# Performance work log

Measured on AMD Instinct MI355X. Metric: run time of the kernel, lower is better.

The kernel has to match this reference:

```python
import jax, jax.numpy as jnp
import numpy as np

B, T, F, H1, H2 = 256, 512, 64, 128, 64


def lstm_seq(x, Wk, Wr, b):
    """Keras-style LSTM with activation='relu', recurrent_activation='sigmoid'.
    x: [B, T, Din]. Returns (all hidden states [B, T, H], last hidden [B, H]).
    Gate order in fused weights is (i, f, g, o) as in Keras."""
    H = Wr.shape[0]
    xT = jnp.swapaxes(x, 0, 1)  # [T, B, Din]
    h0 = jnp.zeros((x.shape[0], H), x.dtype)
    c0 = jnp.zeros((x.shape[0], H), x.dtype)

    def step(carry, xt):
        h, c = carry
        z = xt @ Wk + h @ Wr + b  # [B, 4H]
        i, f, g, o = jnp.split(z, 4, axis=-1)
        i = jax.nn.sigmoid(i)
        f = jax.nn.sigmoid(f)
        o = jax.nn.sigmoid(o)
        g = jax.nn.relu(g)  # activation='relu' replaces tanh
        c = f * c + i * g
        h = o * jax.nn.relu(c)  # relu also applied to cell state output
        return (h, c), h

    (h_last, _), hs = jax.lax.scan(step, (h0, c0), xT)
    return jnp.swapaxes(hs, 0, 1), h_last


def setup_inputs() -> dict:
    key = jax.random.key(0)
    ks = jax.random.split(key, 16)

    def p(k, shape):
        # small init to keep the relu recurrence numerically stable over T=512 steps
        fan_in = shape[0]
        return jax.random.normal(k, shape, dtype=jnp.float32) * (0.5 / np.sqrt(fan_in))

    inp = {
        "x": jax.random.normal(ks[0], (B, T, F), dtype=jnp.float32),
        # encoder layer 1: F -> H1
        "Wk1": p(ks[1], (F, 4 * H1)), "Wr1": p(ks[2], (H1, 4 * H1)), "b1": jnp.zeros((4 * H1,), jnp.float32),
        # encoder layer 2: H1 -> H2 (return last state only)
        "Wk2": p(ks[3], (H1, 4 * H2)), "Wr2": p(ks[4], (H2, 4 * H2)), "b2": jnp.zeros((4 * H2,), jnp.float32),
        # decoder layer 1: H2 -> H2
        "Wd1k": p(ks[5], (H2, 4 * H2)), "Wd1r": p(ks[6], (H2, 4 * H2)), "bd1": jnp.zeros((4 * H2,), jnp.float32),
        # decoder layer 2: H2 -> H1
        "Wd2k": p(ks[7], (H2, 4 * H1)), "Wd2r": p(ks[8], (H1, 4 * H1)), "bd2": jnp.zeros((4 * H1,), jnp.float32),
        # TimeDistributed Dense: H1 -> F
        "Wout": p(ks[9], (H1, F)), "bout": jnp.zeros((F,), jnp.float32),
    }
    return inp


def reference(x, Wk1, Wr1, b1, Wk2, Wr2, b2, Wd1k, Wd1r, bd1, Wd2k, Wd2r, bd2, Wout, bout):
    # Encoder
    h_seq, _ = lstm_seq(x, Wk1, Wr1, b1)            # [B, T, H1]
    _, z = lstm_seq(h_seq, Wk2, Wr2, b2)            # [B, H2] (return_sequences=False)
    # RepeatVector
    z_rep = jnp.broadcast_to(z[:, None, :], (z.shape[0], T, z.shape[1]))  # [B, T, H2]
    # Decoder
    d1, _ = lstm_seq(z_rep, Wd1k, Wd1r, bd1)        # [B, T, H2]
    d2, _ = lstm_seq(d1, Wd2k, Wd2r, bd2)           # [B, T, H1]
    # TimeDistributed Dense
    return d2 @ Wout + bout                          # [B, T, F]
```

## Files before the change

kernel.cpp:

```cpp
#include <hip/hip_runtime.h>

static constexpr int TT = 512;
static constexpr int BB = 256;

#define BARRIER() do { \
    asm volatile("s_waitcnt lgkmcnt(0)" ::: "memory"); \
    __builtin_amdgcn_s_barrier(); \
    asm volatile("" ::: "memory"); \
  } while (0)

__device__ __forceinline__ float sigmoid_fast(float v) {
  const float e = __builtin_amdgcn_exp2f(v * -1.44269504088896340736f);
  return __builtin_amdgcn_rcpf(1.0f + e);
}

__device__ __forceinline__ float dpp_add_xor1(float v) {
  const int p = __builtin_amdgcn_update_dpp(0, __builtin_bit_cast(int, v),
                                            0xB1 , 0xF, 0xF, true);
  return v + __builtin_bit_cast(float, p);
}
__device__ __forceinline__ float dpp_add_xor2(float v) {
  const int p = __builtin_amdgcn_update_dpp(0, __builtin_bit_cast(int, v),
                                            0x4E , 0xF, 0xF, true);
  return v + __builtin_bit_cast(float, p);
}
__device__ __forceinline__ float swz_add_xor4(float v) {
  const int p = __builtin_amdgcn_ds_swizzle(__builtin_bit_cast(int, v), 0x101F);
  return v + __builtin_bit_cast(float, p);
}

template<int DIN, int H, int NSu, bool CONST_X, bool WRITE_SEQ, bool WRITE_LAST, bool FUSE_DENSE>
__global__ void __launch_bounds__(512, 2)
lstm_unit(const float* __restrict__ xin,
          const float* __restrict__ Wk,
          const float* __restrict__ Wr,
          const float* __restrict__ bias,
          float* __restrict__ seq_out,
          float* __restrict__ last_out,
          const float* __restrict__ Wout,
          const float* __restrict__ boutp,
          float* __restrict__ dense_out)
{
  constexpr int NTH  = 512;
  static_assert(H * NSu == NTH, "block = H*NSu = 512");
  constexpr int KTOT = DIN + H;
  constexpr int SL   = KTOT / NSu;
  constexpr int C4H  = 4 * H;
  constexpr int XH   = DIN + H;
  constexpr int NW   = NTH / 64;
  constexpr int UPW  = 64 / NSu;
  constexpr int DK   = FUSE_DENSE ? (H / NW) : 4;
  static_assert(SL * NSu == KTOT && (SL % 4) == 0, "slice float4-able");
  static_assert(NSu == 4 || NSu == 8, "butterfly depth");

  const int tid = (int)threadIdx.x;
  const int b   = (int)blockIdx.x;
  const int l   = tid & 63;
  const int wv  = tid >> 6;
  const int sl  = l & (NSu - 1);
  const int u   = wv * UPW + (l / NSu);

  __shared__ __align__(16) float xh0[XH], xh1[XH];
  __shared__ __align__(16) float dp[2][FUSE_DENSE ? NW * 64 : 4];

  float w[SL * 4];
  #pragma unroll
  for (int i = 0; i < SL; ++i) {
    const int k = sl * SL + i;
    const float* col = (k < DIN) ? &Wk[(size_t)k * C4H] : &Wr[(size_t)(k - DIN) * C4H];
    #pragma unroll
    for (int g = 0; g < 4; ++g) w[i * 4 + g] = col[g * H + u];
  }
  const float bi_ = bias[u], bf_ = bias[H + u], bg_ = bias[2 * H + u], bo_ = bias[3 * H + u];

  float wout_r[DK];
  float boutr = 0.f;
  if constexpr (FUSE_DENSE) {
    #pragma unroll
    for (int j = 0; j < DK; ++j) wout_r[j] = Wout[(size_t)(DK * wv + j) * 64 + l];
    boutr = boutp[l];
  }

  if (tid < H) xh0[DIN + tid] = 0.f;
  if (tid < DIN / 4) {
    const float4 v = *(const float4*)&xin[(CONST_X ? (size_t)b * DIN
                                                   : (size_t)b * TT * DIN) + 4 * tid];
    *((float4*)xh0 + tid) = v;
    if (CONST_X) *((float4*)xh1 + tid) = v;
  }
  BARRIER();

  float cst = 0.f;
  constexpr int TEND = FUSE_DENSE ? TT + 2 : TT;

  for (int t = 0; t < TEND; ++t) {
    float* xc = (t & 1) ? xh1 : xh0;
    float* xn = (t & 1) ? xh0 : xh1;

    float4 xr;
    const bool do_stage = (!CONST_X) && (tid < DIN / 4) && (t + 1 < TT);
    if (do_stage) xr = *(const float4*)&xin[((size_t)b * TT + (t + 1)) * DIN + 4 * tid];

    if (t < TT) {
      const float4* xv = (const float4*)(xc + sl * SL);
      float ai = 0.f, af = 0.f, ag = 0.f, ao = 0.f;
      #pragma unroll
      for (int j = 0; j < SL / 4; ++j) {
        const float4 v = xv[j];
        const float* wj = &w[16 * j];
        ai = fmaf(v.x, wj[0],  ai);  af = fmaf(v.x, wj[1],  af);
        ag = fmaf(v.x, wj[2],  ag);  ao = fmaf(v.x, wj[3],  ao);
        ai = fmaf(v.y, wj[4],  ai);  af = fmaf(v.y, wj[5],  af);
        ag = fmaf(v.y, wj[6],  ag);  ao = fmaf(v.y, wj[7],  ao);
        ai = fmaf(v.z, wj[8],  ai);  af = fmaf(v.z, wj[9],  af);
        ag = fmaf(v.z, wj[10], ag);  ao = fmaf(v.z, wj[11], ao);
        ai = fmaf(v.w, wj[12], ai);  af = fmaf(v.w, wj[13], af);
        ag = fmaf(v.w, wj[14], ag);  ao = fmaf(v.w, wj[15], ao);
      }
      ai = dpp_add_xor1(ai); af = dpp_add_xor1(af);
      ag = dpp_add_xor1(ag); ao = dpp_add_xor1(ao);
      ai = dpp_add_xor2(ai); af = dpp_add_xor2(af);
      ag = dpp_add_xor2(ag); ao = dpp_add_xor2(ao);
      if constexpr (NSu == 8) {
        ai = swz_add_xor4(ai); af = swz_add_xor4(af);
        ag = swz_add_xor4(ag); ao = swz_add_xor4(ao);
      }
      const float gi = sigmoid_fast(ai + bi_);
      const float gf = sigmoid_fast(af + bf_);
      const float go = sigmoid_fast(ao + bo_);
      const float gg = fmaxf(ag + bg_, 0.f);
      cst = fmaf(gf, cst, gi * gg);
      const float h = go * fmaxf(cst, 0.f);
      if (sl == 0) {
        xn[DIN + u] = h;
        if constexpr (WRITE_SEQ)  seq_out[((size_t)b * TT + t) * H + u] = h;
        if constexpr (WRITE_LAST) { if (t == TT - 1) last_out[(size_t)b * H + u] = h; }
      }
    }
    if (do_stage) *((float4*)xn + tid) = xr;

    if constexpr (FUSE_DENSE) {
      if (t >= 1 && t <= TT) {
        const float* hsrc = xc + DIN + DK * wv;
        float a = 0.f;
        #pragma unroll
        for (int j = 0; j < DK; j += 4) {
          const float4 hv = *(const float4*)(hsrc + j);
          a = fmaf(hv.x, wout_r[j + 0], a);
          a = fmaf(hv.y, wout_r[j + 1], a);
          a = fmaf(hv.z, wout_r[j + 2], a);
          a = fmaf(hv.w, wout_r[j + 3], a);
        }
        dp[(t - 1) & 1][wv * 64 + l] = a;
      }
      if (t >= 2 && wv == NW - 1) {
        const float* dq = dp[t & 1];
        float o = boutr;
        #pragma unroll
        for (int j = 0; j < NW; ++j) o += dq[j * 64 + l];
        dense_out[((size_t)b * TT + (t - 2)) * 64 + l] = o;
      }
    }
    if (t < TEND - 1) BARRIER();
  }
}

extern "C" void kernel_launch(void* const* d_in, const int* in_sizes, int n_in,
                              void* d_out, int out_size, void* d_ws, size_t ws_size,
                              hipStream_t stream) {
  const float* x    = (const float*)d_in[0];
  const float* Wk1  = (const float*)d_in[1];
  const float* Wr1  = (const float*)d_in[2];
  const float* b1   = (const float*)d_in[3];
  const float* Wk2  = (const float*)d_in[4];
  const float* Wr2  = (const float*)d_in[5];
  const float* b2   = (const float*)d_in[6];
  const float* Wd1k = (const float*)d_in[7];
  const float* Wd1r = (const float*)d_in[8];
  const float* bd1  = (const float*)d_in[9];
  const float* Wd2k = (const float*)d_in[10];
  const float* Wd2r = (const float*)d_in[11];
  const float* bd2  = (const float*)d_in[12];
  const float* Wout = (const float*)d_in[13];
  const float* bout = (const float*)d_in[14];
  float* out = (float*)d_out;

  const size_t h1_elems = (size_t)BB * TT * 128;
  const size_t need = (h1_elems + (size_t)BB * 64) * sizeof(float);
  if (ws_size < need) return;
  float* h1 = (float*)d_ws;
  float* z  = h1 + h1_elems;
  float* d1 = h1;

  lstm_unit<64, 128, 4, false, true,  false, false><<<BB, 512, 0, stream>>>(
      x,  Wk1,  Wr1,  b1,  h1,      nullptr, nullptr, nullptr, nullptr);
  lstm_unit<128, 64, 8, false, false, true,  false><<<BB, 512, 0, stream>>>(
      h1, Wk2,  Wr2,  b2,  nullptr, z,       nullptr, nullptr, nullptr);
  lstm_unit<64,  64, 8, true,  true,  false, false><<<BB, 512, 0, stream>>>(
      z,  Wd1k, Wd1r, bd1, d1,      nullptr, nullptr, nullptr, nullptr);
  lstm_unit<64, 128, 4, false, false, false, true ><<<BB, 512, 0, stream>>>(
      d1, Wd2k, Wd2r, bd2, nullptr, nullptr, Wout,   bout,    out);
}
```

Measured before the change: 1.422 ms.

## Hoist input projections out of recurrence and fold decoder input GEMM into dec1

Precomputes x@Wk1 for all timesteps with a separate GEMM kernel, so layer 1's recurrent kernel only does h@Wr with a per-step load of precomputed gate inputs. The constant decoder-1 input projection is computed once per batch row. Decoder-1 directly emits d1@Wd2k as precomputed gate inputs for decoder-2, which then also runs recurrence-only. The aim is to shorten each serial step's dot product. In exchange it adds a large workspace buffer and extra global traffic for the precomputed gates, and keeps the old path as a fallback when workspace is small.

```diff
diff --git a/kernel.cpp b/kernel.cpp
--- a/kernel.cpp
+++ b/kernel.cpp
@@ -13,15 +13,14 @@
   const float e = __builtin_amdgcn_exp2f(v * -1.44269504088896340736f);
   return __builtin_amdgcn_rcpf(1.0f + e);
 }
-
 __device__ __forceinline__ float dpp_add_xor1(float v) {
   const int p = __builtin_amdgcn_update_dpp(0, __builtin_bit_cast(int, v),
-                                            0xB1 , 0xF, 0xF, true);
+                                            0xB1, 0xF, 0xF, true);
   return v + __builtin_bit_cast(float, p);
 }
 __device__ __forceinline__ float dpp_add_xor2(float v) {
   const int p = __builtin_amdgcn_update_dpp(0, __builtin_bit_cast(int, v),
-                                            0x4E , 0xF, 0xF, true);
+                                            0x4E, 0xF, 0xF, true);
   return v + __builtin_bit_cast(float, p);
 }
 __device__ __forceinline__ float swz_add_xor4(float v) {
@@ -29,16 +28,259 @@
   return v + __builtin_bit_cast(float, p);
 }
 
+__global__ void __launch_bounds__(512, 2)
+gemm_xk512(const float* __restrict__ A, const float* __restrict__ W,
+           float* __restrict__ C)
+{
+  const int tid = (int)threadIdx.x;
+  const int blk = (int)blockIdx.x;
+  __shared__ __align__(16) float At[128 * 64];
+
+  float w[64];
+  #pragma unroll
+  for (int k = 0; k < 64; ++k) w[k] = W[(size_t)k * 512 + tid];
+
+  const size_t rbase = (size_t)blk * 128;
+  #pragma unroll
+  for (int i = 0; i < 4; ++i)
+    ((float4*)At)[tid + 512 * i] = ((const float4*)(A + rbase * 64))[tid + 512 * i];
+  __syncthreads();
+
+  for (int r = 0; r < 128; ++r) {
+    const float4* ar = (const float4*)(At + r * 64);
+    float a0 = 0.f, a1 = 0.f, a2 = 0.f, a3 = 0.f;
+    #pragma unroll
+    for (int j = 0; j < 16; ++j) {
+      const float4 v = ar[j];
+      a0 = fmaf(v.x, w[4 * j + 0], a0);
+      a1 = fmaf(v.y, w[4 * j + 1], a1);
+      a2 = fmaf(v.z, w[4 * j + 2], a2);
+      a3 = fmaf(v.w, w[4 * j + 3], a3);
+    }
+    C[(rbase + r) * 512 + tid] = (a0 + a1) + (a2 + a3);
+  }
+}
+
+template<bool WRITE_SEQ, bool FUSE_DENSE>
+__global__ void __launch_bounds__(512, 2)
+lstm_rec128(const float* __restrict__ zx,
+            const float* __restrict__ Wr,
+            const float* __restrict__ bias,
+            float* __restrict__ seq_out,
+            const float* __restrict__ Wout,
+            const float* __restrict__ boutp,
+            float* __restrict__ dense_out)
+{
+  constexpr int H = 128, C4H = 512, NW = 8, DK = 16;
+  const int tid = (int)threadIdx.x;
+  const int b   = (int)blockIdx.x;
+  const int l   = tid & 63;
+  const int wv  = tid >> 6;
+  const int sl  = l & 3;
+  const int u   = wv * 16 + (l >> 2);
+
+  __shared__ __align__(16) float hb[2][H];
+  __shared__ __align__(16) float dp[2][FUSE_DENSE ? NW * 64 : 4];
+
+  float w[128];
+  #pragma unroll
+  for (int i = 0; i < 32; ++i) {
+    const float* col = &Wr[(size_t)(sl * 32 + i) * C4H];
+    #pragma unroll
+    for (int g = 0; g < 4; ++g) w[i * 4 + g] = col[g * H + u];
+  }
+  const float bi_ = bias[u], bf_ = bias[H + u], bg_ = bias[2 * H + u], bo_ = bias[3 * H + u];
+
+  float wout_r[FUSE_DENSE ? DK : 1];
+  float boutr = 0.f;
+  if constexpr (FUSE_DENSE) {
+    #pragma unroll
+    for (int j = 0; j < DK; ++j) wout_r[j] = Wout[(size_t)(DK * wv + j) * 64 + l];
+    boutr = boutp[l];
+  }
+
+  if (tid < H) hb[0][tid] = 0.f;
+  const size_t zbase = (size_t)b * TT * C4H + (size_t)sl * H + u;
+  float zq = zx[zbase];
+  BARRIER();
+
+  float cst = 0.f;
+  constexpr int TEND = FUSE_DENSE ? TT + 2 : TT;
+
+  for (int t = 0; t < TEND; ++t) {
+    const int cur = t & 1, nxt = cur ^ 1;
+
+    float zqn;
+    if (t + 1 < TT) zqn = zx[zbase + (size_t)(t + 1) * C4H];
+
+    if (t < TT) {
+      const float4* xv = (const float4*)&hb[cur][sl * 32];
+      float ai = (sl == 0) ? zq : 0.f;
+      float af = (sl == 1) ? zq : 0.f;
+      float ag = (sl == 2) ? zq : 0.f;
+      float ao = (sl == 3) ? zq : 0.f;
+      #pragma unroll
+      for (int j = 0; j < 8; ++j) {
+        const float4 v = xv[j];
+        const float* wj = &w[16 * j];
+        ai = fmaf(v.x, wj[0],  ai);  af = fmaf(v.x, wj[1],  af);
+        ag = fmaf(v.x, wj[2],  ag);  ao = fmaf(v.x, wj[3],  ao);
+        ai = fmaf(v.y, wj[4],  ai);  af = fmaf(v.y, wj[5],  af);
+        ag = fmaf(v.y, wj[6],  ag);  ao = fmaf(v.y, wj[7],  ao);
+        ai = fmaf(v.z, wj[8],  ai);  af = fmaf(v.z, wj[9],  af);
+        ag = fmaf(v.z, wj[10], ag);  ao = fmaf(v.z, wj[11], ao);
+        ai = fmaf(v.w, wj[12], ai);  af = fmaf(v.w, wj[13], af);
+        ag = fmaf(v.w, wj[14], ag);  ao = fmaf(v.w, wj[15], ao);
+      }
+      ai = dpp_add_xor1(ai); af = dpp_add_xor1(af);
+      ag = dpp_add_xor1(ag); ao = dpp_add_xor1(ao);
+      ai = dpp_add_xor2(ai); af = dpp_add_xor2(af);
+      ag = dpp_add_xor2(ag); ao = dpp_add_xor2(ao);
+
+      const float gi = sigmoid_fast(ai + bi_);
+      const float gf = sigmoid_fast(af + bf_);
+      const float go = sigmoid_fast(ao + bo_);
+      const float gg = fmaxf(ag + bg_, 0.f);
+      cst = fmaf(gf, cst, gi * gg);
+      const float h = go * fmaxf(cst, 0.f);
+      if (sl == 0) {
+        hb[nxt][u] = h;
+        if constexpr (WRITE_SEQ) seq_out[((size_t)b * TT + t) * H + u] = h;
+      }
+    }
+
+    if constexpr (FUSE_DENSE) {
+      if (t >= 1 && t <= TT) {
+        const float* hsrc = &hb[cur][DK * wv];
+        float a = 0.f;
+        #pragma unroll
+        for (int j = 0; j < DK; j += 4) {
+          const float4 hv = *(const float4*)(hsrc + j);
+          a = fmaf(hv.x, wout_r[j + 0], a);
+          a = fmaf(hv.y, wout_r[j + 1], a);
+          a = fmaf(hv.z, wout_r[j + 2], a);
+          a = fmaf(hv.w, wout_r[j + 3], a);
+        }
+        dp[(t - 1) & 1][wv * 64 + l] = a;
+      }
+      if (t >= 2 && wv == NW - 1) {
+        const float* dq = dp[t & 1];
+        float o = boutr;
+        #pragma unroll
+        for (int j = 0; j < NW; ++j) o += dq[j * 64 + l];
+        dense_out[((size_t)b * TT + (t - 2)) * 64 + l] = o;
+      }
+    }
+
+    if (t + 1 < TT) zq = zqn;
+    if (t < TEND - 1) BARRIER();
+  }
+}
+
+__global__ void __launch_bounds__(512, 2)
+lstm_dec1_fold(const float* __restrict__ zrow,
+               const float* __restrict__ Wk,
+               const float* __restrict__ Wr,
+               const float* __restrict__ bias,
+               const float* __restrict__ W2,
+               float* __restrict__ zx3)
+{
+  constexpr int H = 64, C4H = 256;
+  const int tid = (int)threadIdx.x;
+  const int b   = (int)blockIdx.x;
+  const int l   = tid & 63;
+  const int wv  = tid >> 6;
+  const int sl  = l & 7;
+  const int u   = wv * 8 + (l >> 3);
+
+  __shared__ __align__(16) float hb[2][H];
+  __shared__ __align__(16) float zl[H];
+
+  float w[32];
+  #pragma unroll
+  for (int i = 0; i < 8; ++i) {
+    const float* col = &Wr[(size_t)(sl * 8 + i) * C4H];
+    #pragma unroll
+    for (int g = 0; g < 4; ++g) w[i * 4 + g] = col[g * H + u];
+  }
+  float w2[64];
+  #pragma unroll
+  for (int k = 0; k < 64; ++k) w2[k] = W2[(size_t)k * 512 + tid];
+  const float bi_ = bias[u], bf_ = bias[H + u], bg_ = bias[2 * H + u], bo_ = bias[3 * H + u];
+
+  if (tid < 16) ((float4*)zl)[tid] = ((const float4*)(zrow + (size_t)b * H))[tid];
+  if (tid < H) hb[0][tid] = 0.f;
+  BARRIER();
+
+  float zi = 0.f, zf = 0.f, zg = 0.f, zo = 0.f;
+  #pragma unroll
+  for (int i = 0; i < 8; ++i) {
+    const int k = sl * 8 + i;
+    const float zv = zl[k];
+    const float* col = &Wk[(size_t)k * C4H];
+    zi = fmaf(zv, col[u],         zi);
+    zf = fmaf(zv, col[H + u],     zf);
+    zg = fmaf(zv, col[2 * H + u], zg);
+    zo = fmaf(zv, col[3 * H + u], zo);
+  }
+
+  float cst = 0.f;
+  for (int t = 0; t < TT + 1; ++t) {
+    const int cur = t & 1, nxt = cur ^ 1;
+    if (t < TT) {
+      const float4* xv = (const float4*)&hb[cur][sl * 8];
+      float ai = zi, af = zf, ag = zg, ao = zo;
+      #pragma unroll
+      for (int j = 0; j < 2; ++j) {
+        const float4 v = xv[j];
+        const float* wj = &w[16 * j];
+        ai = fmaf(v.x, wj[0],  ai);  af = fmaf(v.x, wj[1],  af);
+        ag = fmaf(v.x, wj[2],  ag);  ao = fmaf(v.x, wj[3],  ao);
+        ai = fmaf(v.y, wj[4],  ai);  af = fmaf(v.y, wj[5],  af);
+        ag = fmaf(v.y, wj[6],  ag);  ao = fmaf(v.y, wj[7],  ao);
+        ai = fmaf(v.z, wj[8],  ai);  af = fmaf(v.z, wj[9],  af);
+        ag = fmaf(v.z, wj[10], ag);  ao = fmaf(v.z, wj[11], ao);
+        ai = fmaf(v.w, wj[12], ai);  af = fmaf(v.w, wj[13], af);
+        ag = fmaf(v.w, wj[14], ag);  ao = fmaf(v.w, wj[15], ao);
+      }
+      ai = dpp_add_xor1(ai); af = dpp_add_xor1(af);
+      ag = dpp_add_xor1(ag); ao = dpp_add_xor1(ao);
+      ai = dpp_add_xor2(ai); af = dpp_add_xor2(af);
+      ag = dpp_add_xor2(ag); ao = dpp_add_xor2(ao);
+      ai = swz_add_xor4(ai); af = swz_add_xor4(af);
+      ag = swz_add_xor4(ag); ao = swz_add_xor4(ao);
+
+      const float gi = sigmoid_fast(ai + bi_);
+      const float gf = sigmoid_fast(af + bf_);
+      const float go = sigmoid_fast(ao + bo_);
+      const float gg = fmaxf(ag + bg_, 0.f);
+      cst = fmaf(gf, cst, gi * gg);
+      const float h = go * fmaxf(cst, 0.f);
+      if (sl == 0) hb[nxt][u] = h;
+    }
+    if (t >= 1) {
+      const float* hsrc = hb[cur];
+      float a0 = 0.f, a1 = 0.f, a2 = 0.f, a3 = 0.f;
+      #pragma unroll
+      for (int k = 0; k < 64; k += 4) {
+        const float4 hv = *(const float4*)(hsrc + k);
+        a0 = fmaf(hv.x, w2[k + 0], a0);
+        a1 = fmaf(hv.y, w2[k + 1], a1);
+        a2 = fmaf(hv.z, w2[k + 2], a2);
+        a3 = fmaf(hv.w, w2[k + 3], a3);
+      }
+      zx3[((size_t)b * TT + (t - 1)) * 512 + tid] = (a0 + a1) + (a2 + a3);
+    }
+    if (t < TT) BARRIER();
+  }
+}
+
 template<int DIN, int H, int NSu, bool CONST_X, bool WRITE_SEQ, bool WRITE_LAST, bool FUSE_DENSE>
 __global__ void __launch_bounds__(512, 2)
-lstm_unit(const float* __restrict__ xin,
-          const float* __restrict__ Wk,
-          const float* __restrict__ Wr,
-          const float* __restrict__ bias,
-          float* __restrict__ seq_out,
-          float* __restrict__ last_out,
-          const float* __restrict__ Wout,
-          const float* __restrict__ boutp,
+lstm_unit(const float* __restrict__ xin, const float* __restrict__ Wk,
+          const float* __restrict__ Wr, const float* __restrict__ bias,
+          float* __restrict__ seq_out, float* __restrict__ last_out,
+          const float* __restrict__ Wout, const float* __restrict__ boutp,
           float* __restrict__ dense_out)
 {
   constexpr int NTH  = 512;
@@ -185,19 +427,36 @@
   const float* bout = (const float*)d_in[14];
   float* out = (float*)d_out;
 
-  const size_t h1_elems = (size_t)BB * TT * 128;
-  const size_t need = (h1_elems + (size_t)BB * 64) * sizeof(float);
-  if (ws_size < need) return;
-  float* h1 = (float*)d_ws;
-  float* z  = h1 + h1_elems;
-  float* d1 = h1;
-
-  lstm_unit<64, 128, 4, false, true,  false, false><<<BB, 512, 0, stream>>>(
-      x,  Wk1,  Wr1,  b1,  h1,      nullptr, nullptr, nullptr, nullptr);
-  lstm_unit<128, 64, 8, false, false, true,  false><<<BB, 512, 0, stream>>>(
-      h1, Wk2,  Wr2,  b2,  nullptr, z,       nullptr, nullptr, nullptr);
-  lstm_unit<64,  64, 8, true,  true,  false, false><<<BB, 512, 0, stream>>>(
-      z,  Wd1k, Wd1r, bd1, d1,      nullptr, nullptr, nullptr, nullptr);
-  lstm_unit<64, 128, 4, false, false, false, true ><<<BB, 512, 0, stream>>>(
-      d1, Wd2k, Wd2r, bd2, nullptr, nullptr, Wout,   bout,    out);
-}
+  const size_t BT       = (size_t)BB * TT;
+  const size_t zx_elems = BT * 512;
+  const size_t h1_elems = BT * 128;
+  const size_t need_big   = (zx_elems + h1_elems + (size_t)BB * 64) * sizeof(float);
+  const size_t need_small = (h1_elems + (size_t)BB * 64) * sizeof(float);
+
+  if (ws_size >= need_big) {
+    float* zxA = (float*)d_ws;
+    float* h1  = zxA + zx_elems;
+    float* z   = h1 + h1_elems;
+
+    gemm_xk512<<<(int)(BT / 128), 512, 0, stream>>>(x, Wk1, zxA);
+    lstm_rec128<true, false><<<BB, 512, 0, stream>>>(
+        zxA, Wr1, b1, h1, nullptr, nullptr, nullptr);
+    lstm_unit<128, 64, 8, false, false, true, false><<<BB, 512, 0, stream>>>(
+        h1, Wk2, Wr2, b2, nullptr, z, nullptr, nullptr, nullptr);
+    lstm_dec1_fold<<<BB, 512, 0, stream>>>(z, Wd1k, Wd1r, bd1, Wd2k, zxA);
+    lstm_rec128<false, true><<<BB, 512, 0, stream>>>(
+        zxA, Wd2r, bd2, nullptr, Wout, bout, out);
+  } else if (ws_size >= need_small) {
+    float* h1 = (float*)d_ws;
+    float* z  = h1 + h1_elems;
+    float* d1 = h1;
+    lstm_unit<64, 128, 4, false, true,  false, false><<<BB, 512, 0, stream>>>(
+        x,  Wk1,  Wr1,  b1,  h1,      nullptr, nullptr, nullptr, nullptr);
+    lstm_unit<128, 64, 8, false, false, true,  false><<<BB, 512, 0, stream>>>(
+        h1, Wk2,  Wr2,  b2,  nullptr, z,       nullptr, nullptr, nullptr);
+    lstm_unit<64,  64, 8, true,  true,  false, false><<<BB, 512, 0, stream>>>(
+        z,  Wd1k, Wd1r, bd1, d1,      nullptr, nullptr, nullptr, nullptr);
+    lstm_unit<64, 128, 4, false, false, false, true ><<<BB, 512, 0, stream>>>(
+        d1, Wd2k, Wd2r, bd2, nullptr, nullptr, Wout,   bout,    out);
+  }
+}
```

After: 1.424 ms. Within noise of the previous version (+0.2%).

## Fuse stacked LSTM layers per kernel with chunked input projection pipelining

Applied to the files above, without the earlier changes.

Merges the two encoder LSTMs into one kernel and the two decoder LSTMs plus dense into another. The second layer runs 16 steps behind the first, and the input projections (x@Wk) are computed 8 timesteps at a time, overlapped with the recurrence and staged through shared memory. Only the recurrent weights stay in registers. This removes the global round trip of the intermediate hidden sequences and two kernel launches, and shortens the per-step serial dot product to the recurrent part. In exchange each timestep does more work, register pressure rises, and Wk weights are re-read from global/L2 on every step.

```diff
diff --git a/kernel.cpp b/kernel.cpp
--- a/kernel.cpp
+++ b/kernel.cpp
@@ -13,15 +13,14 @@
   const float e = __builtin_amdgcn_exp2f(v * -1.44269504088896340736f);
   return __builtin_amdgcn_rcpf(1.0f + e);
 }
-
 __device__ __forceinline__ float dpp_add_xor1(float v) {
   const int p = __builtin_amdgcn_update_dpp(0, __builtin_bit_cast(int, v),
-                                            0xB1 , 0xF, 0xF, true);
+                                            0xB1, 0xF, 0xF, true);
   return v + __builtin_bit_cast(float, p);
 }
 __device__ __forceinline__ float dpp_add_xor2(float v) {
   const int p = __builtin_amdgcn_update_dpp(0, __builtin_bit_cast(int, v),
-                                            0x4E , 0xF, 0xF, true);
+                                            0x4E, 0xF, 0xF, true);
   return v + __builtin_bit_cast(float, p);
 }
 __device__ __forceinline__ float swz_add_xor4(float v) {
@@ -29,139 +28,396 @@
   return v + __builtin_bit_cast(float, p);
 }
 
-template<int DIN, int H, int NSu, bool CONST_X, bool WRITE_SEQ, bool WRITE_LAST, bool FUSE_DENSE>
+#define DOT128(XV, W, AI, AF, AG, AO)                                        \
+  _Pragma("unroll")                                                          \
+  for (int jj = 0; jj < 8; ++jj) {                                           \
+    const float4 v = (XV)[jj];                                               \
+    const float* wj = &(W)[16 * jj];                                         \
+    AI = fmaf(v.x, wj[0],  AI);  AF = fmaf(v.x, wj[1],  AF);                 \
+    AG = fmaf(v.x, wj[2],  AG);  AO = fmaf(v.x, wj[3],  AO);                 \
+    AI = fmaf(v.y, wj[4],  AI);  AF = fmaf(v.y, wj[5],  AF);                 \
+    AG = fmaf(v.y, wj[6],  AG);  AO = fmaf(v.y, wj[7],  AO);                 \
+    AI = fmaf(v.z, wj[8],  AI);  AF = fmaf(v.z, wj[9],  AF);                 \
+    AG = fmaf(v.z, wj[10], AG);  AO = fmaf(v.z, wj[11], AO);                 \
+    AI = fmaf(v.w, wj[12], AI);  AF = fmaf(v.w, wj[13], AF);                 \
+    AG = fmaf(v.w, wj[14], AG);  AO = fmaf(v.w, wj[15], AO);                 \
+  }
+
+#define DOT32(XV, W, AI, AF, AG, AO)                                         \
+  _Pragma("unroll")                                                          \
+  for (int jj = 0; jj < 2; ++jj) {                                           \
+    const float4 v = (XV)[jj];                                               \
+    const float* wj = &(W)[16 * jj];                                         \
+    AI = fmaf(v.x, wj[0],  AI);  AF = fmaf(v.x, wj[1],  AF);                 \
+    AG = fmaf(v.x, wj[2],  AG);  AO = fmaf(v.x, wj[3],  AO);                 \
+    AI = fmaf(v.y, wj[4],  AI);  AF = fmaf(v.y, wj[5],  AF);                 \
+    AG = fmaf(v.y, wj[6],  AG);  AO = fmaf(v.y, wj[7],  AO);                 \
+    AI = fmaf(v.z, wj[8],  AI);  AF = fmaf(v.z, wj[9],  AF);                 \
+    AG = fmaf(v.z, wj[10], AG);  AO = fmaf(v.z, wj[11], AO);                 \
+    AI = fmaf(v.w, wj[12], AI);  AF = fmaf(v.w, wj[13], AF);                 \
+    AG = fmaf(v.w, wj[14], AG);  AO = fmaf(v.w, wj[15], AO);                 \
+  }
+
 __global__ void __launch_bounds__(512, 2)
-lstm_unit(const float* __restrict__ xin,
-          const float* __restrict__ Wk,
-          const float* __restrict__ Wr,
-          const float* __restrict__ bias,
-          float* __restrict__ seq_out,
-          float* __restrict__ last_out,
-          const float* __restrict__ Wout,
-          const float* __restrict__ boutp,
-          float* __restrict__ dense_out)
+enc_fused(const float* __restrict__ x,
+          const float* __restrict__ Wk1,
+          const float* __restrict__ Wr1,
+          const float* __restrict__ b1,
+          const float* __restrict__ Wk2,
+          const float* __restrict__ Wr2,
+          const float* __restrict__ b2,
+          float* __restrict__ z_out)
 {
-  constexpr int NTH  = 512;
-  static_assert(H * NSu == NTH, "block = H*NSu = 512");
-  constexpr int KTOT = DIN + H;
-  constexpr int SL   = KTOT / NSu;
-  constexpr int C4H  = 4 * H;
-  constexpr int XH   = DIN + H;
-  constexpr int NW   = NTH / 64;
-  constexpr int UPW  = 64 / NSu;
-  constexpr int DK   = FUSE_DENSE ? (H / NW) : 4;
-  static_assert(SL * NSu == KTOT && (SL % 4) == 0, "slice float4-able");
-  static_assert(NSu == 4 || NSu == 8, "butterfly depth");
-
-  const int tid = (int)threadIdx.x;
-  const int b   = (int)blockIdx.x;
-  const int l   = tid & 63;
-  const int wv  = tid >> 6;
-  const int sl  = l & (NSu - 1);
-  const int u   = wv * UPW + (l / NSu);
-
-  __shared__ __align__(16) float xh0[XH], xh1[XH];
-  __shared__ __align__(16) float dp[2][FUSE_DENSE ? NW * 64 : 4];
-
-  float w[SL * 4];
-  #pragma unroll
-  for (int i = 0; i < SL; ++i) {
-    const int k = sl * SL + i;
-    const float* col = (k < DIN) ? &Wk[(size_t)k * C4H] : &Wr[(size_t)(k - DIN) * C4H];
+  const int tid = (int)threadIdx.x, b = (int)blockIdx.x;
+  const int l  = tid & 63, wv = tid >> 6;
+  const int sl1 = l & 3,  u1 = wv * 16 + (l >> 2);
+  const int sl2 = l & 7,  u2 = wv * 8  + (l >> 3);
+  const int c1 = tid;
+  const int c2 = tid & 255, hf = tid >> 8;
+
+  __shared__ __align__(16) float zx1[2][8][512];
+  __shared__ __align__(16) float h1c[2][8][128];
+  __shared__ __align__(16) float zx2[2][2][8][256];
+  __shared__ __align__(16) float hb2[2][64];
+
+  float w1[128];
+  #pragma unroll
+  for (int i = 0; i < 32; ++i) {
+    const float* col = Wr1 + (size_t)(sl1 * 32 + i) * 512;
     #pragma unroll
-    for (int g = 0; g < 4; ++g) w[i * 4 + g] = col[g * H + u];
-  }
-  const float bi_ = bias[u], bf_ = bias[H + u], bg_ = bias[2 * H + u], bo_ = bias[3 * H + u];
-
-  float wout_r[DK];
-  float boutr = 0.f;
-  if constexpr (FUSE_DENSE) {
+    for (int g = 0; g < 4; ++g) w1[i * 4 + g] = col[g * 128 + u1];
+  }
+  float w2[32];
+  #pragma unroll
+  for (int i = 0; i < 8; ++i) {
+    const float* col = Wr2 + (size_t)(sl2 * 8 + i) * 256;
     #pragma unroll
-    for (int j = 0; j < DK; ++j) wout_r[j] = Wout[(size_t)(DK * wv + j) * 64 + l];
-    boutr = boutp[l];
-  }
-
-  if (tid < H) xh0[DIN + tid] = 0.f;
-  if (tid < DIN / 4) {
-    const float4 v = *(const float4*)&xin[(CONST_X ? (size_t)b * DIN
-                                                   : (size_t)b * TT * DIN) + 4 * tid];
-    *((float4*)xh0 + tid) = v;
-    if (CONST_X) *((float4*)xh1 + tid) = v;
-  }
+    for (int g = 0; g < 4; ++g) w2[i * 4 + g] = col[g * 64 + u2];
+  }
+  const float b1c = b1[c1];
+  const float b2c = (hf == 0) ? b2[c2] : 0.f;
+
+  if (tid < 128) h1c[1][7][tid] = 0.f;
+  if (tid < 64)  hb2[1][tid]    = 0.f;
+
+  float zxa[8], zxa2[8];
+  #pragma unroll
+  for (int r = 0; r < 8; ++r) { zxa[r] = b1c; zxa2[r] = b2c; }
+
+  float cst1 = 0.f, cst2 = 0.f;
+  const float* xb = x + (size_t)b * TT * 64;
   BARRIER();
 
-  float cst = 0.f;
-  constexpr int TEND = FUSE_DENSE ? TT + 2 : TT;
-
-  for (int t = 0; t < TEND; ++t) {
-    float* xc = (t & 1) ? xh1 : xh0;
-    float* xn = (t & 1) ? xh0 : xh1;
-
-    float4 xr;
-    const bool do_stage = (!CONST_X) && (tid < DIN / 4) && (t + 1 < TT);
-    if (do_stage) xr = *(const float4*)&xin[((size_t)b * TT + (t + 1)) * DIN + 4 * tid];
-
-    if (t < TT) {
-      const float4* xv = (const float4*)(xc + sl * SL);
-      float ai = 0.f, af = 0.f, ag = 0.f, ao = 0.f;
-      #pragma unroll
-      for (int j = 0; j < SL / 4; ++j) {
-        const float4 v = xv[j];
-        const float* wj = &w[16 * j];
-        ai = fmaf(v.x, wj[0],  ai);  af = fmaf(v.x, wj[1],  af);
-        ag = fmaf(v.x, wj[2],  ag);  ao = fmaf(v.x, wj[3],  ao);
-        ai = fmaf(v.y, wj[4],  ai);  af = fmaf(v.y, wj[5],  af);
-        ag = fmaf(v.y, wj[6],  ag);  ao = fmaf(v.y, wj[7],  ao);
-        ai = fmaf(v.z, wj[8],  ai);  af = fmaf(v.z, wj[9],  af);
-        ag = fmaf(v.z, wj[10], ag);  ao = fmaf(v.z, wj[11], ao);
-        ai = fmaf(v.w, wj[12], ai);  af = fmaf(v.w, wj[13], af);
-        ag = fmaf(v.w, wj[14], ag);  ao = fmaf(v.w, wj[15], ao);
-      }
+  for (int t = -8; t < 528; ++t) {
+    const int j  = t & 7;
+    const int ch = t >> 3;
+    const bool g1 = (t < 504);
+    const bool g2 = (t >= 8 && t < 520);
+    const bool r1 = (t >= 0 && t < TT);
+    const int  s  = t - 16;
+    const bool r2 = (s >= 0 && s < TT);
+
+    float wk1r[8], wk2r[8];
+    if (g1) {
+      #pragma unroll
+      for (int i = 0; i < 8; ++i) wk1r[i] = Wk1[(size_t)(8 * j + i) * 512 + c1];
+    }
+    if (g2) {
+      #pragma unroll
+      for (int i = 0; i < 8; ++i)
+        wk2r[i] = Wk2[(size_t)(hf * 64 + 8 * j + i) * 256 + c2];
+    }
+
+    if (r1) {
+      const int row = t & 7,        buf  = ch & 1;
+      const int prow = (t - 1) & 7, pbuf = ((t - 1) >> 3) & 1;
+      const float4* xv = (const float4*)&h1c[pbuf][prow][sl1 * 32];
+      const float zq = zx1[buf][row][sl1 * 128 + u1];
+      float ai = (sl1 == 0) ? zq : 0.f;
+      float af = (sl1 == 1) ? zq : 0.f;
+      float ag = (sl1 == 2) ? zq : 0.f;
+      float ao = (sl1 == 3) ? zq : 0.f;
+      DOT128(xv, w1, ai, af, ag, ao);
       ai = dpp_add_xor1(ai); af = dpp_add_xor1(af);
       ag = dpp_add_xor1(ag); ao = dpp_add_xor1(ao);
       ai = dpp_add_xor2(ai); af = dpp_add_xor2(af);
       ag = dpp_add_xor2(ag); ao = dpp_add_xor2(ao);
-      if constexpr (NSu == 8) {
-        ai = swz_add_xor4(ai); af = swz_add_xor4(af);
-        ag = swz_add_xor4(ag); ao = swz_add_xor4(ao);
-      }
-      const float gi = sigmoid_fast(ai + bi_);
-      const float gf = sigmoid_fast(af + bf_);
-      const float go = sigmoid_fast(ao + bo_);
-      const float gg = fmaxf(ag + bg_, 0.f);
-      cst = fmaf(gf, cst, gi * gg);
-      const float h = go * fmaxf(cst, 0.f);
-      if (sl == 0) {
-        xn[DIN + u] = h;
-        if constexpr (WRITE_SEQ)  seq_out[((size_t)b * TT + t) * H + u] = h;
-        if constexpr (WRITE_LAST) { if (t == TT - 1) last_out[(size_t)b * H + u] = h; }
-      }
-    }
-    if (do_stage) *((float4*)xn + tid) = xr;
-
-    if constexpr (FUSE_DENSE) {
-      if (t >= 1 && t <= TT) {
-        const float* hsrc = xc + DIN + DK * wv;
-        float a = 0.f;
+      const float gi = sigmoid_fast(ai);
+      const float gf = sigmoid_fast(af);
+      const float go = sigmoid_fast(ao);
+      const float gg = fmaxf(ag, 0.f);
+      cst1 = fmaf(gf, cst1, gi * gg);
+      const float h = go * fmaxf(cst1, 0.f);
+      if (sl1 == 0) h1c[buf][row][u1] = h;
+    }
+
+    if (r2) {
+      const int row2 = s & 7, buf2 = (s >> 3) & 1;
+      const float4* xv2 = (const float4*)&hb2[(s + 1) & 1][sl2 * 8];
+      float zq2 = 0.f;
+      if (sl2 < 4)
+        zq2 = zx2[buf2][0][row2][sl2 * 64 + u2] + zx2[buf2][1][row2][sl2 * 64 + u2];
+      float ai = (sl2 == 0) ? zq2 : 0.f;
+      float af = (sl2 == 1) ? zq2 : 0.f;
+      float ag = (sl2 == 2) ? zq2 : 0.f;
+      float ao = (sl2 == 3) ? zq2 : 0.f;
+      DOT32(xv2, w2, ai, af, ag, ao);
+      ai = dpp_add_xor1(ai); af = dpp_add_xor1(af);
+      ag = dpp_add_xor1(ag); ao = dpp_add_xor1(ao);
+      ai = dpp_add_xor2(ai); af = dpp_add_xor2(af);
+      ag = dpp_add_xor2(ag); ao = dpp_add_xor2(ao);
+      ai = swz_add_xor4(ai); af = swz_add_xor4(af);
+      ag = swz_add_xor4(ag); ao = swz_add_xor4(ao);
+      const float gi = sigmoid_fast(ai);
+      const float gf = sigmoid_fast(af);
+      const float go = sigmoid_fast(ao);
+      const float gg = fmaxf(ag, 0.f);
+      cst2 = fmaf(gf, cst2, gi * gg);
+      const float h2 = go * fmaxf(cst2, 0.f);
+      if (sl2 == 0) {
+        hb2[s & 1][u2] = h2;
+        if (s == TT - 1) z_out[(size_t)b * 64 + u2] = h2;
+      }
+    }
+
+    if (g1) {
+      const float* base = xb + (size_t)(8 * (ch + 1)) * 64 + 8 * j;
+      #pragma unroll
+      for (int rg = 0; rg < 2; ++rg) {
+        float4 xq[8];
         #pragma unroll
-        for (int j = 0; j < DK; j += 4) {
-          const float4 hv = *(const float4*)(hsrc + j);
-          a = fmaf(hv.x, wout_r[j + 0], a);
-          a = fmaf(hv.y, wout_r[j + 1], a);
-          a = fmaf(hv.z, wout_r[j + 2], a);
-          a = fmaf(hv.w, wout_r[j + 3], a);
+        for (int rr = 0; rr < 4; ++rr) {
+          const float* p = base + (rg * 4 + rr) * 64;
+          xq[2 * rr]     = *(const float4*)p;
+          xq[2 * rr + 1] = *(const float4*)(p + 4);
         }
-        dp[(t - 1) & 1][wv * 64 + l] = a;
-      }
-      if (t >= 2 && wv == NW - 1) {
-        const float* dq = dp[t & 1];
-        float o = boutr;
         #pragma unroll
-        for (int j = 0; j < NW; ++j) o += dq[j * 64 + l];
-        dense_out[((size_t)b * TT + (t - 2)) * 64 + l] = o;
-      }
-    }
-    if (t < TEND - 1) BARRIER();
+        for (int rr = 0; rr < 4; ++rr) {
+          float a = zxa[rg * 4 + rr];
+          a = fmaf(xq[2*rr].x,   wk1r[0], a);
+          a = fmaf(xq[2*rr].y,   wk1r[1], a);
+          a = fmaf(xq[2*rr].z,   wk1r[2], a);
+          a = fmaf(xq[2*rr].w,   wk1r[3], a);
+          a = fmaf(xq[2*rr+1].x, wk1r[4], a);
+          a = fmaf(xq[2*rr+1].y, wk1r[5], a);
+          a = fmaf(xq[2*rr+1].z, wk1r[6], a);
+          a = fmaf(xq[2*rr+1].w, wk1r[7], a);
+          zxa[rg * 4 + rr] = a;
+        }
+      }
+      if (j == 7) {
+        #pragma unroll
+        for (int r = 0; r < 8; ++r) {
+          zx1[(ch + 1) & 1][r][c1] = zxa[r];
+          zxa[r] = b1c;
+        }
+      }
+    }
+
+    if (g2) {
+      const int cc = ch - 1;
+      #pragma unroll
+      for (int r = 0; r < 8; ++r) {
+        const float4 ha = *(const float4*)&h1c[cc & 1][r][hf * 64 + 8 * j];
+        const float4 hbq = *(const float4*)&h1c[cc & 1][r][hf * 64 + 8 * j + 4];
+        float a = zxa2[r];
+        a = fmaf(ha.x,  wk2r[0], a);
+        a = fmaf(ha.y,  wk2r[1], a);
+        a = fmaf(ha.z,  wk2r[2], a);
+        a = fmaf(ha.w,  wk2r[3], a);
+        a = fmaf(hbq.x, wk2r[4], a);
+        a = fmaf(hbq.y, wk2r[5], a);
+        a = fmaf(hbq.z, wk2r[6], a);
+        a = fmaf(hbq.w, wk2r[7], a);
+        zxa2[r] = a;
+      }
+      if (j == 7) {
+        #pragma unroll
+        for (int r = 0; r < 8; ++r) {
+          zx2[cc & 1][hf][r][c2] = zxa2[r];
+          zxa2[r] = b2c;
+        }
+      }
+    }
+
+    if (t < 527) BARRIER();
+  }
+}
+
+__global__ void __launch_bounds__(512, 2)
+dec_fused(const float* __restrict__ zrow,
+          const float* __restrict__ Wd1k,
+          const float* __restrict__ Wd1r,
+          const float* __restrict__ bd1,
+          const float* __restrict__ Wd2k,
+          const float* __restrict__ Wd2r,
+          const float* __restrict__ bd2,
+          const float* __restrict__ Wout,
+          const float* __restrict__ boutp,
+          float* __restrict__ out)
+{
+  const int tid = (int)threadIdx.x, b = (int)blockIdx.x;
+  const int l  = tid & 63, wv = tid >> 6;
+  const int sl1 = l & 3,  u1 = wv * 16 + (l >> 2);
+  const int sl2 = l & 7,  u2 = wv * 8  + (l >> 3);
+  const int c3 = tid;
+
+  __shared__ __align__(16) float zx3[2][8][512];
+  __shared__ __align__(16) float hd1c[2][8][64];
+  __shared__ __align__(16) float hb2d[2][128];
+  __shared__ __align__(16) float dp[2][512];
+  __shared__ __align__(16) float zl[64];
+
+  float w[32];
+  #pragma unroll
+  for (int i = 0; i < 8; ++i) {
+    const float* col = Wd1r + (size_t)(sl2 * 8 + i) * 256;
+    #pragma unroll
+    for (int g = 0; g < 4; ++g) w[i * 4 + g] = col[g * 64 + u2];
+  }
+  float w1[128];
+  #pragma unroll
+  for (int i = 0; i < 32; ++i) {
+    const float* col = Wd2r + (size_t)(sl1 * 32 + i) * 512;
+    #pragma unroll
+    for (int g = 0; g < 4; ++g) w1[i * 4 + g] = col[g * 128 + u1];
+  }
+  float wout_r[16];
+  #pragma unroll
+  for (int jj = 0; jj < 16; ++jj) wout_r[jj] = Wout[(size_t)(16 * wv + jj) * 64 + l];
+  const float boutr = boutp[l];
+  const float bd2c = bd2[c3];
+
+  if (tid < 16) ((float4*)zl)[tid] = ((const float4*)(zrow + (size_t)b * 64))[tid];
+  if (tid < 64)  hd1c[1][7][tid] = 0.f;
+  if (tid < 128) hb2d[1][tid]   = 0.f;
+  float zxa3[8];
+  #pragma unroll
+  for (int r = 0; r < 8; ++r) zxa3[r] = bd2c;
+  BARRIER();
+
+  float zi = (sl2 == 0) ? bd1[u2]        : 0.f;
+  float zf = (sl2 == 0) ? bd1[64 + u2]   : 0.f;
+  float zg = (sl2 == 0) ? bd1[128 + u2]  : 0.f;
+  float zo = (sl2 == 0) ? bd1[192 + u2]  : 0.f;
+  #pragma unroll
+  for (int i = 0; i < 8; ++i) {
+    const int k = sl2 * 8 + i;
+    const float zv = zl[k];
+    const float* col = Wd1k + (size_t)k * 256;
+    zi = fmaf(zv, col[u2],        zi);
+    zf = fmaf(zv, col[64 + u2],   zf);
+    zg = fmaf(zv, col[128 + u2],  zg);
+    zo = fmaf(zv, col[192 + u2],  zo);
+  }
+
+  float cst1 = 0.f, cst2 = 0.f;
+
+  for (int t = -8; t < 530; ++t) {
+    const int j  = t & 7;
+    const int ch = t >> 3;
+    const bool rd1 = (t >= 0 && t < TT);
+    const bool g3  = (t >= 8 && t < 520);
+    const int  s   = t - 16;
+    const bool rd2 = (s >= 0 && s < TT);
+
+    float wk3r[8];
+    if (g3) {
+      #pragma unroll
+      for (int i = 0; i < 8; ++i) wk3r[i] = Wd2k[(size_t)(8 * j + i) * 512 + c3];
+    }
+
+    if (rd1) {
+      const int row = t & 7,        buf  = ch & 1;
+      const int prow = (t - 1) & 7, pbuf = ((t - 1) >> 3) & 1;
+      const float4* xv = (const float4*)&hd1c[pbuf][prow][sl2 * 8];
+      float ai = zi, af = zf, ag = zg, ao = zo;
+      DOT32(xv, w, ai, af, ag, ao);
+      ai = dpp_add_xor1(ai); af = dpp_add_xor1(af);
+      ag = dpp_add_xor1(ag); ao = dpp_add_xor1(ao);
+      ai = dpp_add_xor2(ai); af = dpp_add_xor2(af);
+      ag = dpp_add_xor2(ag); ao = dpp_add_xor2(ao);
+      ai = swz_add_xor4(ai); af = swz_add_xor4(af);
+      ag = swz_add_xor4(ag); ao = swz_add_xor4(ao);
+      const float gi = sigmoid_fast(ai);
+      const float gf = sigmoid_fast(af);
+      const float go = sigmoid_fast(ao);
+      const float gg = fmaxf(ag, 0.f);
+      cst1 = fmaf(gf, cst1, gi * gg);
+      const float h = go * fmaxf(cst1, 0.f);
+      if (sl2 == 0) hd1c[buf][row][u2] = h;
+    }
+
+    if (rd2) {
+      const int row2 = s & 7, buf2 = (s >> 3) & 1;
+      const float4* xv2 = (const float4*)&hb2d[(s + 1) & 1][sl1 * 32];
+      const float zq = zx3[buf2][row2][sl1 * 128 + u1];
+      float ai = (sl1 == 0) ? zq : 0.f;
+      float af = (sl1 == 1) ? zq : 0.f;
+      float ag = (sl1 == 2) ? zq : 0.f;
+      float ao = (sl1 == 3) ? zq : 0.f;
+      DOT128(xv2, w1, ai, af, ag, ao);
+      ai = dpp_add_xor1(ai); af = dpp_add_xor1(af);
+      ag = dpp_add_xor1(ag); ao = dpp_add_xor1(ao);
+      ai = dpp_add_xor2(ai); af = dpp_add_xor2(af);
+      ag = dpp_add_xor2(ag); ao = dpp_add_xor2(ao);
+      const float gi = sigmoid_fast(ai);
+      const float gf = sigmoid_fast(af);
+      const float go = sigmoid_fast(ao);
+      const float gg = fmaxf(ag, 0.f);
+      cst2 = fmaf(gf, cst2, gi * gg);
+      const float h2 = go * fmaxf(cst2, 0.f);
+      if (sl1 == 0) hb2d[s & 1][u1] = h2;
+    }
+
+    if (s >= 1 && s <= TT) {
+      const float* hsrc = &hb2d[(s + 1) & 1][16 * wv];
+      float a = 0.f;
+      #pragma unroll
+      for (int q = 0; q < 16; q += 4) {
+        const float4 hv = *(const float4*)(hsrc + q);
+        a = fmaf(hv.x, wout_r[q + 0], a);
+        a = fmaf(hv.y, wout_r[q + 1], a);
+        a = fmaf(hv.z, wout_r[q + 2], a);
+        a = fmaf(hv.w, wout_r[q + 3], a);
+      }
+      dp[(s - 1) & 1][wv * 64 + l] = a;
+    }
+    if (s >= 2 && s <= TT + 1 && wv == 7) {
+      const float* dq = dp[s & 1];
+      float o = boutr;
+      #pragma unroll
+      for (int q = 0; q < 8; ++q) o += dq[q * 64 + l];
+      out[((size_t)b * TT + (s - 2)) * 64 + l] = o;
+    }
+
+    if (g3) {
+      const int cc = ch - 1;
+      #pragma unroll
+      for (int r = 0; r < 8; ++r) {
+        const float4 ha  = *(const float4*)&hd1c[cc & 1][r][8 * j];
+        const float4 hbq = *(const float4*)&hd1c[cc & 1][r][8 * j + 4];
+        float a = zxa3[r];
+        a = fmaf(ha.x,  wk3r[0], a);
+        a = fmaf(ha.y,  wk3r[1], a);
+        a = fmaf(ha.z,  wk3r[2], a);
+        a = fmaf(ha.w,  wk3r[3], a);
+        a = fmaf(hbq.x, wk3r[4], a);
+        a = fmaf(hbq.y, wk3r[5], a);
+        a = fmaf(hbq.z, wk3r[6], a);
+        a = fmaf(hbq.w, wk3r[7], a);
+        zxa3[r] = a;
+      }
+      if (j == 7) {
+        #pragma unroll
+        for (int r = 0; r < 8; ++r) {
+          zx3[cc & 1][r][c3] = zxa3[r];
+          zxa3[r] = bd2c;
+        }
+      }
+    }
+
+    if (t < 529) BARRIER();
   }
 }
 
@@ -185,19 +441,10 @@
   const float* bout = (const float*)d_in[14];
   float* out = (float*)d_out;
 
-  const size_t h1_elems = (size_t)BB * TT * 128;
-  const size_t need = (h1_elems + (size_t)BB * 64) * sizeof(float);
-  if (ws_size < need) return;
-  float* h1 = (float*)d_ws;
-  float* z  = h1 + h1_elems;
-  float* d1 = h1;
-
-  lstm_unit<64, 128, 4, false, true,  false, false><<<BB, 512, 0, stream>>>(
-      x,  Wk1,  Wr1,  b1,  h1,      nullptr, nullptr, nullptr, nullptr);
-  lstm_unit<128, 64, 8, false, false, true,  false><<<BB, 512, 0, stream>>>(
-      h1, Wk2,  Wr2,  b2,  nullptr, z,       nullptr, nullptr, nullptr);
-  lstm_unit<64,  64, 8, true,  true,  false, false><<<BB, 512, 0, stream>>>(
-      z,  Wd1k, Wd1r, bd1, d1,      nullptr, nullptr, nullptr, nullptr);
-  lstm_unit<64, 128, 4, false, false, false, true ><<<BB, 512, 0, stream>>>(
-      d1, Wd2k, Wd2r, bd2, nullptr, nullptr, Wout,   bout,    out);
-}
+  if (ws_size < (size_t)BB * 64 * sizeof(float)) return;
+  float* z = (float*)d_ws;
+
+  enc_fused<<<BB, 512, 0, stream>>>(x, Wk1, Wr1, b1, Wk2, Wr2, b2, z);
+  dec_fused<<<BB, 512, 0, stream>>>(z, Wd1k, Wd1r, bd1, Wd2k, Wd2r, bd2,
+                                    Wout, bout, out);
+}
```

Result: slower. 1.839 ms (+29.3%).
